# Optimization experiments

Hardware: AMD Instinct MI355X
Metric: run time of the kernel (lower is better)

Reference implementation:

```python
import jax, jax.numpy as jnp
import numpy as np

N = 8192   # number of nodes / relationships
D = 64     # input_dim == output_dim


def setup_inputs() -> dict:
    key = jax.random.key(0)
    ks = jax.random.split(key, 13)
    s = 0.05
    return {
        "object_features": jax.random.normal(ks[0], (N, D), dtype=jnp.float32),
        "relationship_features": jax.random.normal(ks[1], (N, D), dtype=jnp.float32),
        # sparse-ish 0/1 adjacency, as in the reference usage
        "adjacency_matrix": (jax.random.uniform(ks[2], (N, N)) < 0.05).astype(jnp.float32),
        # nn.Linear params, stored as [in, out] (i.e. torch weight transposed)
        "W_obj": jax.random.normal(ks[3], (D, D), dtype=jnp.float32) * s,
        "b_obj": jax.random.normal(ks[4], (D,), dtype=jnp.float32) * s,
        "W_nobj": jax.random.normal(ks[5], (D, D), dtype=jnp.float32) * s,
        "b_nobj": jax.random.normal(ks[6], (D,), dtype=jnp.float32) * s,
        "W_rel": jax.random.normal(ks[7], (D, D), dtype=jnp.float32) * s,
        "b_rel": jax.random.normal(ks[8], (D,), dtype=jnp.float32) * s,
        "W_skip": jax.random.normal(ks[9], (D, D), dtype=jnp.float32) * s,
        "b_skip": jax.random.normal(ks[10], (D,), dtype=jnp.float32) * s,
        "Wa_w": jax.random.normal(ks[11], (2 * D, 1), dtype=jnp.float32) * s,  # Linear(2D -> 1)
        "Wa_b": jax.random.normal(ks[12], (1,), dtype=jnp.float32) * s,
    }


def reference(object_features, relationship_features, adjacency_matrix,
              W_obj, b_obj, W_nobj, b_nobj, W_rel, b_rel,
              W_skip, b_skip, Wa_w, Wa_b):
    x, r, A = object_features, relationship_features, adjacency_matrix
    d = x.shape[1]

    # message projections (small GEMMs)
    msgs_obj = x @ W_obj + b_obj                      # [N, D]
    msgs_nbr = A.T @ (x @ W_nobj + b_nobj)            # [N, D]
    msgs_rel = r @ W_rel + b_rel                      # [N, D]
    aggregated = msgs_obj + msgs_nbr + msgs_rel       # [N, D]

    # Wa(concat([x_i, r_j])) = x_i @ Wa_w[:d] + r_j @ Wa_w[d:] + Wa_b
    # (avoids materializing the [N, N, 2D] concat the torch code builds)
    sx = x @ Wa_w[:d]                                 # [N, 1] (per row i)
    sr = r @ Wa_w[d:]                                 # [N, 1] (per col j)
    scores = (sx + sr.T + Wa_b) * A                   # [N, N], masked-by-multiply
    attention = jax.nn.softmax(scores, axis=1)        # [N, N]

    # sum_j attn[i, j] * aggregated[i, :]  (exactly the torch broadcast-sum over dim=1)
    attn_agg = jnp.einsum('ij,ik->ik', attention, aggregated)  # [N, D]

    return x @ W_skip + b_skip + attn_agg
```

## Files before the change

kernel.cpp:

```cpp
#include <hip/hip_runtime.h>

typedef __attribute__((ext_vector_type(8))) short short8;
typedef __attribute__((ext_vector_type(4))) float f32x4;

#define NN 8192
#define DD 64

__device__ inline unsigned short f2bf(float f){
  unsigned b = __float_as_uint(f);
  b = (b + 0x7fffu + ((b >> 16) & 1u)) >> 16;
  return (unsigned short)b;
}

__device__ __forceinline__ void glds16(const void* g, void* l){
  __builtin_amdgcn_global_load_lds((const __attribute__((address_space(1))) void*)g,
                                   (__attribute__((address_space(3))) void*)l, 16, 0, 0);
}


__global__ __launch_bounds__(256) void k_proj(
    const float* __restrict__ x, const float* __restrict__ r,
    const float* __restrict__ Wobj,  const float* __restrict__ bobj,
    const float* __restrict__ Wnobj, const float* __restrict__ bnobj,
    const float* __restrict__ Wrel,  const float* __restrict__ brel,
    const float* __restrict__ Wskip, const float* __restrict__ bskip,
    float* __restrict__ accT, unsigned short* __restrict__ yT)
{
  const int i  = blockIdx.x * 256 + threadIdx.x;
  const int d0 = blockIdx.y * 8;

  float ay[8], az[8];
#pragma unroll
  for (int t = 0; t < 8; t++){ ay[t] = 0.f; az[t] = 0.f; }

  const float4* xp = (const float4*)(x + (size_t)i * DD);
  const float4* rp = (const float4*)(r + (size_t)i * DD);

#pragma unroll
  for (int kb = 0; kb < 4; kb++){
    float xv[16], rv[16];
#pragma unroll
    for (int p = 0; p < 4; p++){
      float4 u = xp[kb*4 + p];
      xv[4*p+0]=u.x; xv[4*p+1]=u.y; xv[4*p+2]=u.z; xv[4*p+3]=u.w;
      float4 v = rp[kb*4 + p];
      rv[4*p+0]=v.x; rv[4*p+1]=v.y; rv[4*p+2]=v.z; rv[4*p+3]=v.w;
    }
#pragma unroll
    for (int kk = 0; kk < 16; kk++){
      const int wb = (kb*16 + kk) * DD + d0;
      const float xk = xv[kk], rk = rv[kk];
#pragma unroll
      for (int t = 0; t < 8; t++){
        ay[t] += xk * Wnobj[wb + t];
        az[t] += xk * Wobj [wb + t];
        az[t] += xk * Wskip[wb + t];
        az[t] += rk * Wrel [wb + t];
      }
    }
  }

#pragma unroll
  for (int t = 0; t < 8; t++){
    ay[t] += bnobj[d0 + t];
    az[t] += bobj[d0 + t] + brel[d0 + t] + bskip[d0 + t];
    yT[(size_t)(d0 + t) * NN + i]   = f2bf(ay[t]);
    accT[(size_t)(d0 + t) * NN + i] = az[t];
  }
}

#define BN 128
#define KSPLIT 8
#define KCH (NN / KSPLIT)
#define KT 32
#define NIT (KCH / KT)
#define ATILE (KT * BN)
#define YPITCH 40
#define YSZ (DD * YPITCH)

__global__ __launch_bounds__(256) void k_spmm(
    const float* __restrict__ A,
    const unsigned short* __restrict__ yT,
    unsigned short* __restrict__ partb)
{
  __shared__ float Af[2 * ATILE];
  __shared__ short Ylds[2 * YSZ];

  const int tid  = threadIdx.x;
  const int lane = tid & 63;
  const int wave = tid >> 6;
  const int q    = lane >> 4;
  const int nn   = lane & 15;

  const int j0     = blockIdx.x * BN;
  const int kstart = blockIdx.y * KCH;

  const int cY = tid & 3;
  const int m  = tid >> 2;
  const unsigned short* yp = yT + (size_t)m * NN + kstart + cY * 8;

  const int arow0 = lane >> 5;
  const int ac    = ((lane & 31) ^ (4 * wave)) << 2;
  const float* abase = A + (size_t)kstart * NN + j0 + ac;

  uint4 ybuf;
  auto issue = [&](int buf, int it){
    const float* at = abase + (size_t)(it * KT) * NN;
    float* ldsb = &Af[buf * ATILE];
#pragma unroll
    for (int p = 0; p < 4; p++){
      const int k0 = wave * 8 + p * 2;
      glds16(at + (size_t)(k0 + arow0) * NN, ldsb + k0 * BN);
    }
    ybuf = *(const uint4*)(yp + (size_t)it * KT);
  };
  auto stageY = [&](int buf){
    *(uint4*)(&Ylds[buf * YSZ + m * YPITCH + cY * 8]) = ybuf;
  };

  f32x4 acc[4][2];
#pragma unroll
  for (int a = 0; a < 4; a++)
#pragma unroll
    for (int b = 0; b < 2; b++)
      acc[a][b] = (f32x4){0.f, 0.f, 0.f, 0.f};

  issue(0, 0);
  stageY(0);
  __syncthreads();

  for (int it = 0; it < NIT; ++it){
    if (it + 1 < NIT) issue((it + 1) & 1, it + 1);
    const unsigned short* Ab = (const unsigned short*)&Af[(it & 1) * ATILE];
    const short* Yb = &Ylds[(it & 1) * YSZ];

    short8 af[4];
#pragma unroll
    for (int mt = 0; mt < 4; mt++)
      af[mt] = *(const short8*)(&Yb[(mt*16 + nn) * YPITCH + q*8]);
#pragma unroll
    for (int nt = 0; nt < 2; nt++){
      const int col = wave * 32 + nt * 16 + nn;
      const unsigned short* bp =
          Ab + (q*8) * 256 + (((col >> 2) ^ (4*q)) * 8) + (col & 3) * 2 + 1;
      short8 bf;
#pragma unroll
      for (int jj = 0; jj < 8; jj++) bf[jj] = (short)bp[jj * 256];
#pragma unroll
      for (int mt = 0; mt < 4; mt++)
        acc[mt][nt] = __builtin_amdgcn_mfma_f32_16x16x32_bf16(af[mt], bf, acc[mt][nt], 0, 0, 0);
    }

    if (it + 1 < NIT){
      stageY((it + 1) & 1);
      __syncthreads();
    }
  }

  unsigned short* pp = partb + (size_t)blockIdx.y * DD * NN;
#pragma unroll
  for (int mt = 0; mt < 4; mt++)
#pragma unroll
    for (int nt = 0; nt < 2; nt++)
#pragma unroll
      for (int v = 0; v < 4; v++){
        const int d   = mt * 16 + q * 4 + v;
        const int col = j0 + wave * 32 + nt * 16 + nn;
        pp[(size_t)d * NN + col] = f2bf(acc[mt][nt][v]);
      }
}

__global__ __launch_bounds__(256) void k_out(
    const float* __restrict__ accT, const unsigned short* __restrict__ partb,
    float* __restrict__ out)
{
  __shared__ float t[32][65];
  const int tid = threadIdx.x;
  const int jb  = blockIdx.x * 64;
  const int dh  = blockIdx.y * 32;

#pragma unroll
  for (int rep = 0; rep < 4; rep++){
    const int dl = rep * 8 + (tid >> 5);
    const int j2 = (tid & 31) * 2;
    const size_t base = (size_t)(dh + dl) * NN + jb + j2;
    const float2 a2 = *(const float2*)(accT + base);
    float sx = a2.x, sy = a2.y;
#pragma unroll
    for (int kb = 0; kb < KSPLIT; kb++){
      const unsigned v = __builtin_nontemporal_load(
          (const unsigned*)(partb + (size_t)kb * DD * NN + base));
      sx += __uint_as_float((v & 0xFFFFu) << 16);
      sy += __uint_as_float(v & 0xFFFF0000u);
    }
    t[dl][j2] = sx; t[dl][j2 + 1] = sy;
  }
  __syncthreads();
#pragma unroll
  for (int pass = 0; pass < 8; pass++){
    const int j  = pass * 8 + (tid >> 5);
    const int dl = tid & 31;
    out[(size_t)(jb + j) * DD + dh + dl] = t[dl][j];
  }
}

extern "C" void kernel_launch(void* const* d_in, const int* in_sizes, int n_in,
                              void* d_out, int out_size, void* d_ws, size_t ws_size,
                              hipStream_t stream) {
  const float* x     = (const float*)d_in[0];
  const float* r     = (const float*)d_in[1];
  const float* A     = (const float*)d_in[2];
  const float* Wobj  = (const float*)d_in[3];
  const float* bobj  = (const float*)d_in[4];
  const float* Wnobj = (const float*)d_in[5];
  const float* bnobj = (const float*)d_in[6];
  const float* Wrel  = (const float*)d_in[7];
  const float* brel  = (const float*)d_in[8];
  const float* Wskip = (const float*)d_in[9];
  const float* bskip = (const float*)d_in[10];

  char* ws = (char*)d_ws;
  float* accT         = (float*)ws;
  unsigned short* yT  = (unsigned short*)(ws + (size_t)DD*NN*4);
  unsigned short* pb  = (unsigned short*)(ws + 3u*1024*1024);

  k_proj<<<dim3(32, 8), 256, 0, stream>>>(x, r, Wobj, bobj, Wnobj, bnobj,
                                          Wrel, brel, Wskip, bskip, accT, yT);
  k_spmm<<<dim3(NN / BN, KSPLIT), 256, 0, stream>>>(A, yT, pb);
  k_out<<<dim3(NN / 64, 2), 256, 0, stream>>>(accT, pb, (float*)d_out);
}
```

Measured before the change: 408.4 us.

## Triple-buffer SpMM loads with explicit vmcnt waits and split projection outputs

The SpMM kernel moves from double to triple buffering of the A tile and Y slice in LDS. It issues loads two iterations ahead and uses manual s_waitcnt vmcnt/lgkmcnt plus raw s_barrier instead of __syncthreads, so more global loads stay in flight. The projection kernel now computes 4 output columns per thread over twice as many blocks, giving more parallelism and lower register pressure. The cost is more LDS per block, which may lower occupancy, and the hand-counted waitcnt values are fragile.

```diff
diff --git a/kernel.cpp b/kernel.cpp
--- a/kernel.cpp
+++ b/kernel.cpp
@@ -27,12 +27,9 @@
     float* __restrict__ accT, unsigned short* __restrict__ yT)
 {
   const int i  = blockIdx.x * 256 + threadIdx.x;
-  const int d0 = blockIdx.y * 8;
-
-  float ay[8], az[8];
-#pragma unroll
-  for (int t = 0; t < 8; t++){ ay[t] = 0.f; az[t] = 0.f; }
-
+  const int d0 = blockIdx.y * 4;
+
+  float ay[4] = {0.f,0.f,0.f,0.f}, az[4] = {0.f,0.f,0.f,0.f};
   const float4* xp = (const float4*)(x + (size_t)i * DD);
   const float4* rp = (const float4*)(r + (size_t)i * DD);
 
@@ -51,7 +48,7 @@
       const int wb = (kb*16 + kk) * DD + d0;
       const float xk = xv[kk], rk = rv[kk];
 #pragma unroll
-      for (int t = 0; t < 8; t++){
+      for (int t = 0; t < 4; t++){
         ay[t] += xk * Wnobj[wb + t];
         az[t] += xk * Wobj [wb + t];
         az[t] += xk * Wskip[wb + t];
@@ -61,7 +58,7 @@
   }
 
 #pragma unroll
-  for (int t = 0; t < 8; t++){
+  for (int t = 0; t < 4; t++){
     ay[t] += bnobj[d0 + t];
     az[t] += bobj[d0 + t] + brel[d0 + t] + bskip[d0 + t];
     yT[(size_t)(d0 + t) * NN + i]   = f2bf(ay[t]);
@@ -83,8 +80,8 @@
     const unsigned short* __restrict__ yT,
     unsigned short* __restrict__ partb)
 {
-  __shared__ float Af[2 * ATILE];
-  __shared__ short Ylds[2 * YSZ];
+  __shared__ float Af[3 * ATILE];
+  __shared__ short Ylds[3 * YSZ];
 
   const int tid  = threadIdx.x;
   const int lane = tid & 63;
@@ -103,19 +100,19 @@
   const int ac    = ((lane & 31) ^ (4 * wave)) << 2;
   const float* abase = A + (size_t)kstart * NN + j0 + ac;
 
-  uint4 ybuf;
-  auto issue = [&](int buf, int it){
+  auto issue = [&](int slot, int it) -> uint4 {
+    uint4 y = *(const uint4*)(yp + (size_t)it * KT);
     const float* at = abase + (size_t)(it * KT) * NN;
-    float* ldsb = &Af[buf * ATILE];
+    float* ldsb = &Af[slot * ATILE];
 #pragma unroll
     for (int p = 0; p < 4; p++){
       const int k0 = wave * 8 + p * 2;
       glds16(at + (size_t)(k0 + arow0) * NN, ldsb + k0 * BN);
     }
-    ybuf = *(const uint4*)(yp + (size_t)it * KT);
+    return y;
   };
-  auto stageY = [&](int buf){
-    *(uint4*)(&Ylds[buf * YSZ + m * YPITCH + cY * 8]) = ybuf;
+  auto stageY = [&](int slot, uint4 v){
+    *(uint4*)(&Ylds[slot * YSZ + m * YPITCH + cY * 8]) = v;
   };
 
   f32x4 acc[4][2];
@@ -125,14 +122,28 @@
     for (int b = 0; b < 2; b++)
       acc[a][b] = (f32x4){0.f, 0.f, 0.f, 0.f};
 
-  issue(0, 0);
-  stageY(0);
-  __syncthreads();
+  uint4 ycur = issue(0, 0);
+  asm volatile("" ::: "memory");
+  uint4 ynxt = issue(1, 1);
+  asm volatile("s_waitcnt vmcnt(5)" ::: "memory");
+  stageY(0, ycur);
+  ycur = ynxt;
+  asm volatile("s_waitcnt lgkmcnt(0)" ::: "memory");
+  __builtin_amdgcn_s_barrier();
 
   for (int it = 0; it < NIT; ++it){
-    if (it + 1 < NIT) issue((it + 1) & 1, it + 1);
-    const unsigned short* Ab = (const unsigned short*)&Af[(it & 1) * ATILE];
-    const short* Yb = &Ylds[(it & 1) * YSZ];
+    if (it + 2 < NIT){
+      ynxt = issue((it + 2) % 3, it + 2);
+      asm volatile("s_waitcnt vmcnt(5)" ::: "memory");
+      stageY((it + 1) % 3, ycur);
+      ycur = ynxt;
+    } else if (it + 1 < NIT){
+      asm volatile("s_waitcnt vmcnt(0)" ::: "memory");
+      stageY((it + 1) % 3, ycur);
+    }
+
+    const unsigned short* Ab = (const unsigned short*)&Af[(it % 3) * ATILE];
+    const short* Yb = &Ylds[(it % 3) * YSZ];
 
     short8 af[4];
 #pragma unroll
@@ -152,8 +163,8 @@
     }
 
     if (it + 1 < NIT){
-      stageY((it + 1) & 1);
-      __syncthreads();
+      asm volatile("s_waitcnt lgkmcnt(0)" ::: "memory");
+      __builtin_amdgcn_s_barrier();
     }
   }
 
@@ -224,8 +235,8 @@
   unsigned short* yT  = (unsigned short*)(ws + (size_t)DD*NN*4);
   unsigned short* pb  = (unsigned short*)(ws + 3u*1024*1024);
 
-  k_proj<<<dim3(32, 8), 256, 0, stream>>>(x, r, Wobj, bobj, Wnobj, bnobj,
-                                          Wrel, brel, Wskip, bskip, accT, yT);
+  k_proj<<<dim3(32, 16), 256, 0, stream>>>(x, r, Wobj, bobj, Wnobj, bnobj,
+                                           Wrel, brel, Wskip, bskip, accT, yT);
   k_spmm<<<dim3(NN / BN, KSPLIT), 256, 0, stream>>>(A, yT, pb);
   k_out<<<dim3(NN / 64, 2), 256, 0, stream>>>(accT, pb, (float*)d_out);
 }
```

Result: no change. 407.4 us (-0.2%).
